# Optimization experiments

Measured on AMD Instinct MI355X. Metric: run time of the kernel, lower is better.

Reference implementation:

```python
import jax, jax.numpy as jnp
import numpy as np

HEAD, DIM_IN, HDIM = 8, 256, 64
B, N = 4, 2048


def setup_inputs() -> dict:
    key = jax.random.key(0)
    k1, k2, k3, k4 = jax.random.split(key, 4)
    # xavier_uniform gain=1.414 bounds
    def xavier(k, shape, fan_in, fan_out):
        bound = 1.414 * np.sqrt(6.0 / (fan_in + fan_out))
        return jax.random.uniform(k, shape, jnp.float32, -bound, bound)
    h = jax.random.normal(k1, (B, N, DIM_IN), jnp.float32)
    w = xavier(k2, (HEAD, DIM_IN, HDIM), DIM_IN, HDIM)
    a_src = xavier(k3, (HEAD, HDIM, 1), HDIM, 1)
    a_dst = xavier(k4, (HEAD, HDIM, 1), HDIM, 1)
    b = jnp.zeros((HDIM,), jnp.float32)
    return {"h": h, "w": w, "a_src": a_src, "a_dst": a_dst, "b": b}


def reference(h, w, a_src, a_dst, b):
    # h: [B,N,Din], w: [H,Din,O] -> h_: [B,H,N,O]
    h_ = jnp.einsum("bnd,hdo->bhno", h, w)
    # additive attention logits per node: [B,H,N]
    src = jnp.einsum("bhno,ho->bhn", h_, a_src[..., 0])
    dst = jnp.einsum("bhno,ho->bhn", h_, a_dst[..., 0])
    # attn[b,h,i,j] = leaky_relu(src[i] + dst[j]); softmax over j
    logits = jax.nn.leaky_relu(src[..., :, None] + dst[..., None, :], negative_slope=0.2)
    attn = jax.nn.softmax(logits, axis=-1)  # [B,H,N,N]
    h_out = jnp.einsum("bhij,bhjo->bhio", attn, h_)
    return h_out + b
```

## Files before the change

kernel.cpp:

```cpp
#include <hip/hip_runtime.h>
#include <cstdint>
#include <cstddef>


#define HEADS 8
#define DIN   256
#define HDIM  64
#define NN    2048

typedef __attribute__((ext_vector_type(8))) _Float16 f16x8;
typedef __attribute__((ext_vector_type(2))) _Float16 f16x2;
typedef __attribute__((ext_vector_type(2))) __fp16   fp16x2;
typedef __attribute__((ext_vector_type(4))) float f32x4;

union H8 { f16x8 v; f16x2 p[4]; unsigned u[4]; };
union F2U { f16x2 h; fp16x2 q; unsigned u; };

__device__ __forceinline__ f16x2 pkrtz(float a, float b) {
  F2U t; t.q = __builtin_amdgcn_cvt_pkrtz(a, b);
  return t.h;
}
__device__ __forceinline__ unsigned pkrtz_u(float a, float b) {
  F2U t; t.q = __builtin_amdgcn_cvt_pkrtz(a, b);
  return t.u;
}

__global__ __launch_bounds__(256) void gat_wt(const float* __restrict__ w,
                                              _Float16* __restrict__ wt) {
  const int idx = blockIdx.x * 256 + threadIdx.x;
  const int o  = idx & 63;
  const int k  = (idx >> 6) & 255;
  const int hd = idx >> 14;
  wt[(hd * HDIM + o) * DIN + k] = (_Float16)w[idx];
}

__global__ __launch_bounds__(256) void gat_hc(const float* __restrict__ h,
                                              _Float16* __restrict__ hc) {
  const int idx = blockIdx.x * 256 + threadIdx.x;
  const float* p = h + (size_t)idx * 8;
  float4 x0 = ((const float4*)p)[0];
  float4 x1 = ((const float4*)p)[1];
  H8 o;
  o.p[0] = pkrtz(x0.x, x0.y); o.p[1] = pkrtz(x0.z, x0.w);
  o.p[2] = pkrtz(x1.x, x1.y); o.p[3] = pkrtz(x1.z, x1.w);
  *(f16x8*)(hc + (size_t)idx * 8) = o.v;
}

__global__ __launch_bounds__(256) void gat_proj(const _Float16* __restrict__ hc,
                                                const _Float16* __restrict__ wt,
                                                const float* __restrict__ a_src,
                                                const float* __restrict__ a_dst,
                                                _Float16* __restrict__ h_t,
                                                float* __restrict__ src_s,
                                                float* __restrict__ dst_s) {
  const int head = blockIdx.x;
  const int rt   = blockIdx.y;
  const int tid  = threadIdx.x;
  const int w    = tid >> 6;
  const int lane = tid & 63;
  const int l15  = lane & 15, lg = lane >> 4;

  const int rowg = rt * 128 + w * 32;
  const _Float16* hb = hc + (size_t)rowg * DIN;
  const _Float16* wb = wt + head * (HDIM * DIN);

  f32x4 acc[2][4] = {};
#pragma unroll
  for (int kk = 0; kk < 8; ++kk) {
    const int k0 = kk * 32 + lg * 8;
    f16x8 af[2];
#pragma unroll
    for (int m = 0; m < 2; ++m)
      af[m] = *(const f16x8*)(hb + (size_t)(m * 16 + l15) * DIN + k0);
    f16x8 bfr[4];
#pragma unroll
    for (int n = 0; n < 4; ++n)
      bfr[n] = *(const f16x8*)(wb + (size_t)(n * 16 + l15) * DIN + k0);
#pragma unroll
    for (int m = 0; m < 2; ++m)
#pragma unroll
      for (int n = 0; n < 4; ++n)
        acc[m][n] = __builtin_amdgcn_mfma_f32_16x16x32_f16(af[m], bfr[n], acc[m][n], 0, 0, 0);
  }

  const int b   = (rt * 128) >> 11;
  const int nl0 = ((rt * 128) & 2047) + w * 32;
  const int bh  = b * HEADS + head;
  _Float16* hb_t = h_t + (size_t)bh * (256 * 512);
#pragma unroll
  for (int m = 0; m < 2; ++m)
#pragma unroll
    for (int n = 0; n < 4; ++n) {
      uint2 pk;
      pk.x = pkrtz_u(acc[m][n][0], acc[m][n][1]);
      pk.y = pkrtz_u(acc[m][n][2], acc[m][n][3]);
      const int j0 = nl0 + m * 16 + lg * 4;
      const int o  = n * 16 + l15;
      *(uint2*)(hb_t + (size_t)(j0 >> 3) * 512 + o * 8 + (j0 & 7)) = pk;
    }

  const float LOG2E = 1.4426950408889634f;
  float as4[4], ad4[4];
#pragma unroll
  for (int n = 0; n < 4; ++n) {
    as4[n] = a_src[head * HDIM + n * 16 + l15];
    ad4[n] = a_dst[head * HDIM + n * 16 + l15];
  }
#pragma unroll
  for (int m = 0; m < 2; ++m)
#pragma unroll
    for (int reg = 0; reg < 4; ++reg) {
      float ps = 0.f, pd = 0.f;
#pragma unroll
      for (int n = 0; n < 4; ++n) {
        float c = acc[m][n][reg];
        ps = fmaf(c, as4[n], ps);
        pd = fmaf(c, ad4[n], pd);
      }
#pragma unroll
      for (int off = 1; off <= 8; off <<= 1) {
        ps += __shfl_xor(ps, off);
        pd += __shfl_xor(pd, off);
      }
      if (l15 == 0) {
        const int nl = nl0 + m * 16 + lg * 4 + reg;
        src_s[(size_t)bh * NN + nl] = ps * LOG2E;
        dst_s[(size_t)bh * NN + nl] = pd * LOG2E;
      }
    }
}

__global__ __launch_bounds__(256) void gat_flash(const float* __restrict__ src_s,
                                                 const float* __restrict__ dst_s,
                                                 const _Float16* __restrict__ h_t,
                                                 const float* __restrict__ bias,
                                                 float* __restrict__ out) {
  const int it  = blockIdx.x;
  const int bh  = blockIdx.y;
  const int tid = threadIdx.x;
  const int w   = tid >> 6;
  const int lane = tid & 63;
  const int l15 = lane & 15, lg = lane >> 4;

  __shared__ _Float16 Ef[NN];
  __shared__ _Float16 Ff[NN];
  __shared__ float red[4];

  const float* dstp = dst_s + (size_t)bh * NN;

  float d[8];
  {
    float4 q0 = *(const float4*)(dstp + tid * 8);
    float4 q1 = *(const float4*)(dstp + tid * 8 + 4);
    d[0]=q0.x; d[1]=q0.y; d[2]=q0.z; d[3]=q0.w;
    d[4]=q1.x; d[5]=q1.y; d[6]=q1.z; d[7]=q1.w;
  }
  float dm = fmaxf(fmaxf(fmaxf(d[0],d[1]),fmaxf(d[2],d[3])),
                   fmaxf(fmaxf(d[4],d[5]),fmaxf(d[6],d[7])));
#pragma unroll
  for (int off = 32; off >= 1; off >>= 1) dm = fmaxf(dm, __shfl_xor(dm, off));
  if (lane == 0) red[w] = dm;
  __syncthreads();
  dm = fmaxf(fmaxf(red[0], red[1]), fmaxf(red[2], red[3]));

  {
    H8 e8, f8;
#pragma unroll
    for (int k = 0; k < 4; ++k) {
      float a0 = d[2*k]   - dm;
      float a1 = d[2*k+1] - dm;
      e8.p[k] = pkrtz(__builtin_amdgcn_exp2f(a0), __builtin_amdgcn_exp2f(a1));
      f8.p[k] = pkrtz(__builtin_amdgcn_exp2f(0.2f * a0),
                      __builtin_amdgcn_exp2f(0.2f * a1));
    }
    *(f16x8*)(&Ef[tid * 8]) = e8.v;
    *(f16x8*)(&Ff[tid * 8]) = f8.v;
  }
  __syncthreads();

  const float* srcp = src_s + (size_t)bh * NN + it * 128 + w * 32;
  f16x2 u2[2], v2[2];
#pragma unroll
  for (int m = 0; m < 2; ++m) {
    float sv   = srcp[m * 16 + l15];
    float smax = sv + dm;
    float mi   = fmaxf(smax, 0.2f * smax);
    float u    = __builtin_amdgcn_exp2f(smax - mi);
    float v    = __builtin_amdgcn_exp2f(fmaf(0.2f, smax, -mi));
    u2[m] = pkrtz(u, u);
    v2[m] = pkrtz(v, v);
  }

  f32x4 acc[2][4] = {};
  f32x4 accs[2]   = {};
  H8 onesU; onesU.u[0] = onesU.u[1] = onesU.u[2] = onesU.u[3] = 0x3C003C00u;
  const f16x8 ones = onesU.v;

  const _Float16* fb = h_t + (size_t)bh * (256 * 512) + lg * 512 + l15 * 8;

#define LOADF(P, jc) do {                                              \
    const _Float16* fp_ = fb + (size_t)(jc) * 2048;                    \
    P##0 = *(const f16x8*)(fp_);                                       \
    P##1 = *(const f16x8*)(fp_ + 128);                                 \
    P##2 = *(const f16x8*)(fp_ + 256);                                 \
    P##3 = *(const f16x8*)(fp_ + 384);                                 \
    P##e = *(const f16x8*)(&Ef[(jc) * 32 + lg * 8]);                   \
    P##f = *(const f16x8*)(&Ff[(jc) * 32 + lg * 8]);                   \
  } while (0)

#define FLASH_STEP(B0_, B1_, B2_, B3_, E_, F_) do {                    \
    H8 eu_, fu_; eu_.v = E_; fu_.v = F_;                               \
    _Pragma("unroll") for (int m = 0; m < 2; ++m) {                    \
      H8 af_;                                                          \
      af_.p[0] = __builtin_elementwise_max(u2[m] * eu_.p[0], v2[m] * fu_.p[0]); \
      af_.p[1] = __builtin_elementwise_max(u2[m] * eu_.p[1], v2[m] * fu_.p[1]); \
      af_.p[2] = __builtin_elementwise_max(u2[m] * eu_.p[2], v2[m] * fu_.p[2]); \
      af_.p[3] = __builtin_elementwise_max(u2[m] * eu_.p[3], v2[m] * fu_.p[3]); \
      acc[m][0] = __builtin_amdgcn_mfma_f32_16x16x32_f16(af_.v, B0_, acc[m][0], 0, 0, 0); \
      acc[m][1] = __builtin_amdgcn_mfma_f32_16x16x32_f16(af_.v, B1_, acc[m][1], 0, 0, 0); \
      acc[m][2] = __builtin_amdgcn_mfma_f32_16x16x32_f16(af_.v, B2_, acc[m][2], 0, 0, 0); \
      acc[m][3] = __builtin_amdgcn_mfma_f32_16x16x32_f16(af_.v, B3_, acc[m][3], 0, 0, 0); \
      accs[m]   = __builtin_amdgcn_mfma_f32_16x16x32_f16(af_.v, ones, accs[m], 0, 0, 0);  \
    }                                                                  \
  } while (0)

  f16x8 A0, A1, A2, A3, B0, B1, B2, B3;
  f16x8 Ae, Af, Be, Bf;

  LOADF(A, 0);
#pragma unroll 1
  for (int jc2 = 0; jc2 < 31; ++jc2) {
    LOADF(B, 2 * jc2 + 1);
    FLASH_STEP(A0, A1, A2, A3, Ae, Af);
    LOADF(A, 2 * jc2 + 2);
    FLASH_STEP(B0, B1, B2, B3, Be, Bf);
  }
  LOADF(B, 63);
  FLASH_STEP(A0, A1, A2, A3, Ae, Af);
  FLASH_STEP(B0, B1, B2, B3, Be, Bf);

#undef LOADF
#undef FLASH_STEP

  float bb[4];
#pragma unroll
  for (int n = 0; n < 4; ++n) bb[n] = bias[n * 16 + l15];

  float* ob = out + ((size_t)bh * NN + it * 128 + w * 32) * HDIM;
#pragma unroll
  for (int m = 0; m < 2; ++m)
#pragma unroll
    for (int reg = 0; reg < 4; ++reg) {
      const float linv = 1.0f / accs[m][reg];
      const int r = m * 16 + lg * 4 + reg;
#pragma unroll
      for (int n = 0; n < 4; ++n)
        ob[(size_t)r * HDIM + n * 16 + l15] = fmaf(acc[m][n][reg], linv, bb[n]);
    }
}

extern "C" void kernel_launch(void* const* d_in, const int* in_sizes, int n_in,
                              void* d_out, int out_size, void* d_ws, size_t ws_size,
                              hipStream_t stream) {
  const float* h     = (const float*)d_in[0];
  const float* w     = (const float*)d_in[1];
  const float* a_src = (const float*)d_in[2];
  const float* a_dst = (const float*)d_in[3];
  const float* bias  = (const float*)d_in[4];
  float* out = (float*)d_out;

  char* ws = (char*)d_ws;
  _Float16* wt  = (_Float16*)ws;
  _Float16* h_t = (_Float16*)(ws + 262144);
  float* src_s = (float*)(ws + 262144 + 8388608);
  float* dst_s = (float*)(ws + 262144 + 8388608 + 262144);

  _Float16* hcv = (_Float16*)d_out;

  hipLaunchKernelGGL(gat_wt,    dim3(512),    dim3(256), 0, stream, w, wt);
  hipLaunchKernelGGL(gat_hc,    dim3(1024),   dim3(256), 0, stream, h, hcv);
  hipLaunchKernelGGL(gat_proj,  dim3(8, 64),  dim3(256), 0, stream,
                     hcv, wt, a_src, a_dst, h_t, src_s, dst_s);
  hipLaunchKernelGGL(gat_flash, dim3(16, 32), dim3(256), 0, stream,
                     src_s, dst_s, h_t, bias, out);
}
```

Before: 60.50 us.

## Stage V panels cooperatively through double-buffered shared memory in flash loop

Each block now loads the 2048-half V chunk for every step with one cooperative 16-byte load per thread into a double-buffered LDS tile, rather than having each wave read its own copies directly from global memory. This cuts redundant global/L2 traffic across the four waves. In exchange it adds a __syncthreads per iteration and LDS reads for the B operands, which may serialize waves and reduce the latency hiding the previous register prefetch provided.

Measured after the change: 62.28 us. 3.0% more time.

```diff
diff --git a/kernel.cpp b/kernel.cpp
--- a/kernel.cpp
+++ b/kernel.cpp
@@ -144,9 +144,13 @@
 
   __shared__ _Float16 Ef[NN];
   __shared__ _Float16 Ff[NN];
+  __shared__ _Float16 Vt[2][2048];
   __shared__ float red[4];
 
   const float* dstp = dst_s + (size_t)bh * NN;
+  const _Float16* vpan = h_t + (size_t)bh * (256 * 512);
+
+  f16x8 vreg = *(const f16x8*)(vpan + tid * 8);
 
   float d[8];
   {
@@ -176,6 +180,7 @@
     *(f16x8*)(&Ef[tid * 8]) = e8.v;
     *(f16x8*)(&Ff[tid * 8]) = f8.v;
   }
+  *(f16x8*)(&Vt[0][tid * 8]) = vreg;
   __syncthreads();
 
   const float* srcp = src_s + (size_t)bh * NN + it * 128 + w * 32;
@@ -196,20 +201,15 @@
   H8 onesU; onesU.u[0] = onesU.u[1] = onesU.u[2] = onesU.u[3] = 0x3C003C00u;
   const f16x8 ones = onesU.v;
 
-  const _Float16* fb = h_t + (size_t)bh * (256 * 512) + lg * 512 + l15 * 8;
-
-#define LOADF(P, jc) do {                                              \
-    const _Float16* fp_ = fb + (size_t)(jc) * 2048;                    \
-    P##0 = *(const f16x8*)(fp_);                                       \
-    P##1 = *(const f16x8*)(fp_ + 128);                                 \
-    P##2 = *(const f16x8*)(fp_ + 256);                                 \
-    P##3 = *(const f16x8*)(fp_ + 384);                                 \
-    P##e = *(const f16x8*)(&Ef[(jc) * 32 + lg * 8]);                   \
-    P##f = *(const f16x8*)(&Ff[(jc) * 32 + lg * 8]);                   \
-  } while (0)
-
-#define FLASH_STEP(B0_, B1_, B2_, B3_, E_, F_) do {                    \
-    H8 eu_, fu_; eu_.v = E_; fu_.v = F_;                               \
+#define FLASH_STEP(buf, jc) do {                                       \
+    const _Float16* vb_ = &Vt[buf][lg * 512 + l15 * 8];                \
+    f16x8 B0_ = *(const f16x8*)(vb_);                                  \
+    f16x8 B1_ = *(const f16x8*)(vb_ + 128);                            \
+    f16x8 B2_ = *(const f16x8*)(vb_ + 256);                            \
+    f16x8 B3_ = *(const f16x8*)(vb_ + 384);                            \
+    H8 eu_, fu_;                                                       \
+    eu_.v = *(const f16x8*)(&Ef[(jc) * 32 + lg * 8]);                  \
+    fu_.v = *(const f16x8*)(&Ff[(jc) * 32 + lg * 8]);                  \
     _Pragma("unroll") for (int m = 0; m < 2; ++m) {                    \
       H8 af_;                                                          \
       af_.p[0] = __builtin_elementwise_max(u2[m] * eu_.p[0], v2[m] * fu_.p[0]); \
@@ -224,22 +224,15 @@
     }                                                                  \
   } while (0)
 
-  f16x8 A0, A1, A2, A3, B0, B1, B2, B3;
-  f16x8 Ae, Af, Be, Bf;
-
-  LOADF(A, 0);
 #pragma unroll 1
-  for (int jc2 = 0; jc2 < 31; ++jc2) {
-    LOADF(B, 2 * jc2 + 1);
-    FLASH_STEP(A0, A1, A2, A3, Ae, Af);
-    LOADF(A, 2 * jc2 + 2);
-    FLASH_STEP(B0, B1, B2, B3, Be, Bf);
-  }
-  LOADF(B, 63);
-  FLASH_STEP(A0, A1, A2, A3, Ae, Af);
-  FLASH_STEP(B0, B1, B2, B3, Be, Bf);
-
-#undef LOADF
+  for (int t = 0; t < 63; ++t) {
+    f16x8 vnext = *(const f16x8*)(vpan + (size_t)(t + 1) * 2048 + tid * 8);
+    FLASH_STEP(t & 1, t);
+    *(f16x8*)(&Vt[(t + 1) & 1][tid * 8]) = vnext;
+    __syncthreads();
+  }
+  FLASH_STEP(1, 63);
+
 #undef FLASH_STEP
 
   float bb[4];
```
